# Kernel tuning notes

Hardware: AMD Instinct MI355X
Metric: run time of the kernel (lower is better)

The kernel has to match this reference:

```python
import jax, jax.numpy as jnp
import numpy as np

DIM = 768
NUM_HEADS = 12
HEAD_DIM = DIM // NUM_HEADS
SCALE = HEAD_DIM ** -0.5


def setup_inputs() -> dict:
    key = jax.random.key(0)
    k_x, k_qkv, k_pw, k_pb = jax.random.split(key, 4)
    x = jax.random.normal(k_x, (1, 4096, DIM), dtype=jnp.float32)
    # nn.Linear weights stored as [out, in]; apply as x @ W.T
    w_qkv = jax.random.normal(k_qkv, (3 * DIM, DIM), dtype=jnp.float32) * (DIM ** -0.5)
    w_proj = jax.random.normal(k_pw, (DIM, DIM), dtype=jnp.float32) * (DIM ** -0.5)
    b_proj = jax.random.normal(k_pb, (DIM,), dtype=jnp.float32) * 0.01
    return {"x": x, "w_qkv": w_qkv, "w_proj": w_proj, "b_proj": b_proj}


def reference(x, w_qkv, w_proj, b_proj):
    b, s, d = x.shape
    qkv = jnp.einsum('bsd,ed->bse', x, w_qkv)            # [B,S,3D]
    qkv = qkv.reshape(b, s, 3, NUM_HEADS, HEAD_DIM)
    qkv = jnp.transpose(qkv, (2, 0, 3, 1, 4))            # [3,B,H,S,hd]
    q, k, v = qkv[0], qkv[1], qkv[2]
    scores = jnp.einsum('bhqe,bhke->bhqk', q, k) * SCALE  # [B,H,S,S]
    probs = jax.nn.softmax(scores, axis=-1)
    attended = jnp.einsum('bhqk,bhke->bhqe', probs, v)    # [B,H,S,hd]
    attended = jnp.transpose(attended, (0, 2, 1, 3)).reshape(b, s, d)
    return jnp.einsum('bsd,ed->bse', attended, w_proj) + b_proj
```

## Files before the change

### kernel.cpp

```cpp
#include <hip/hip_runtime.h>
#include <hip/hip_bf16.h>

using short8 = __attribute__((ext_vector_type(8))) short;
using s16x4  = __attribute__((ext_vector_type(4))) short;
using f32x4  = __attribute__((ext_vector_type(4))) float;
using f32x16 = __attribute__((ext_vector_type(16))) float;
using v2i    = __attribute__((ext_vector_type(2))) int;

#define DIM   768
#define D3    2304
#define SEQL  4096
#define NHEAD 12
#define NSPLIT 2

#if defined(__has_builtin)
#  if __has_builtin(__builtin_amdgcn_permlane32_swap)
#    define HAVE_PLSWAP 1
#  endif
#endif

static __device__ __forceinline__ short f2bs(float f) {
  union { __hip_bfloat16 h; short s; } u;
  u.h = __float2bfloat16(f);
  return u.s;
}

static __device__ __forceinline__ float bf2f(short s) {
  union { unsigned u; float f; } x;
  x.u = ((unsigned)(unsigned short)s) << 16;
  return x.f;
}

static __device__ __forceinline__ int cvtpk(float lo, float hi) {
  int r;
  asm("v_cvt_pk_bf16_f32 %0, %1, %2" : "=v"(r) : "v"(lo), "v"(hi));
  return r;
}

static __device__ __forceinline__ float ex2(float x) {
  float r;
  asm("v_exp_f32 %0, %1" : "=v"(r) : "v"(x));
  return r;
}

static __device__ __forceinline__ void gl_lds16(const void* g, void* lds) {
  __builtin_amdgcn_global_load_lds((const __attribute__((address_space(1))) void*)g,
                                   (__attribute__((address_space(3))) void*)lds, 16, 0, 0);
}

__global__ __launch_bounds__(256) void cvt_kernel(const float* __restrict__ src,
                                                  short* __restrict__ dst,
                                                  int n, int nscaled) {
  int i = (blockIdx.x * 256 + threadIdx.x) * 4;
  if (i >= n) return;
  f32x4 v = *(const f32x4*)(src + i);
  float sc = (i < nscaled) ? 0.125f * 1.4426950408889634f : 1.0f;
  s16x4 o;
  #pragma unroll
  for (int j = 0; j < 4; ++j) o[j] = f2bs(v[j] * sc);
  *(s16x4*)(dst + i) = o;
}

template <bool BF16OUT>
__global__ __launch_bounds__(256) void gemm_bt(const short* __restrict__ A,
                                               const short* __restrict__ B,
                                               short* __restrict__ Cb,
                                               float* __restrict__ Cf,
                                               const float* __restrict__ bias,
                                               int M, int N, int K) {
  __shared__ short As[128 * 64];
  __shared__ short Bs[128 * 64];
  const int tid = threadIdx.x;
  const int l  = tid & 63;
  const int w  = tid >> 6;
  const int g  = l >> 4, lc = l & 15;
  const int wr = w >> 1, wc = w & 1;
  const int m0 = blockIdx.y * 128, n0 = blockIdx.x * 128;
  const int trow = tid >> 3;
  const int tcol = (tid & 7) * 8;

  f32x4 acc[4][4];
  #pragma unroll
  for (int a = 0; a < 4; ++a)
    #pragma unroll
    for (int b = 0; b < 4; ++b) acc[a][b] = (f32x4){0.f, 0.f, 0.f, 0.f};

  for (int k0 = 0; k0 < K; k0 += 64) {
    __syncthreads();
    #pragma unroll
    for (int i = 0; i < 4; ++i) {
      int row = i * 32 + trow;
      gl_lds16(A + (size_t)(m0 + row) * K + k0 + tcol, As + row * 64 + tcol);
      gl_lds16(B + (size_t)(n0 + row) * K + k0 + tcol, Bs + row * 64 + tcol);
    }
    __syncthreads();
    #pragma unroll
    for (int kk = 0; kk < 2; ++kk) {
      short8 af[4], bf[4];
      #pragma unroll
      for (int mt = 0; mt < 4; ++mt)
        af[mt] = *(const short8*)(As + (wr * 64 + mt * 16 + lc) * 64 + kk * 32 + g * 8);
      #pragma unroll
      for (int nt = 0; nt < 4; ++nt)
        bf[nt] = *(const short8*)(Bs + (wc * 64 + nt * 16 + lc) * 64 + kk * 32 + g * 8);
      #pragma unroll
      for (int mt = 0; mt < 4; ++mt)
        #pragma unroll
        for (int nt = 0; nt < 4; ++nt)
          acc[mt][nt] = __builtin_amdgcn_mfma_f32_16x16x32_bf16(af[mt], bf[nt], acc[mt][nt], 0, 0, 0);
    }
  }

  #pragma unroll
  for (int mt = 0; mt < 4; ++mt)
    #pragma unroll
    for (int nt = 0; nt < 4; ++nt)
      #pragma unroll
      for (int r = 0; r < 4; ++r) {
        int row = m0 + wr * 64 + mt * 16 + g * 4 + r;
        int col = n0 + wc * 64 + nt * 16 + lc;
        float v = acc[mt][nt][r];
        if (BF16OUT) Cb[(size_t)row * N + col] = f2bs(v);
        else         Cf[(size_t)row * N + col] = v + bias[col];
      }
}

__global__ __launch_bounds__(256) void transpose_v(const short* __restrict__ qkv,
                                                   short* __restrict__ vtg) {
  __shared__ short T[64][72];
  const int jt = blockIdx.x, hd = blockIdx.y, tid = threadIdx.x;
  #pragma unroll
  for (int i = 0; i < 2; ++i) {
    int idx = i * 256 + tid;
    int r = idx >> 3, c = idx & 7;
    *(short8*)&T[r][8 * c] =
        *(const short8*)(qkv + (size_t)(jt * 64 + r) * D3 + 1536 + hd * 64 + 8 * c);
  }
  __syncthreads();
  #pragma unroll
  for (int i = 0; i < 2; ++i) {
    int idx = i * 256 + tid;
    int d = idx >> 3, jc = idx & 7;
    short8 v;
    #pragma unroll
    for (int e = 0; e < 8; ++e) v[e] = T[8 * jc + e][d];
    *(short8*)(vtg + ((size_t)hd * 64 + d) * 4096 + jt * 64 + 8 * jc) = v;
  }
}

__global__ __launch_bounds__(256) void attn_kernel(const short* __restrict__ qkv,
                                                   const short* __restrict__ vtg,
                                                   short* __restrict__ O0,
                                                   short* __restrict__ O1,
                                                   float* __restrict__ Lp,
                                                   int tpb) {
  __shared__ short Ks[2][64 * 64];
  __shared__ short Vt[2][64 * 64];

  const int tid = threadIdx.x;
  const int l = tid & 63, w = tid >> 6;
  const int h = l >> 5;
  const int q5 = l & 31;
  const int head = blockIdx.y;
  const int hoff = head * 64;
  const int qbase = blockIdx.x * 128 + w * 32;
  const int z = blockIdx.z;
  const int t0 = z * tpb;

  short8 qf[4];
  {
    const short* qrow = qkv + (size_t)(qbase + q5) * D3 + hoff;
    #pragma unroll
    for (int ks = 0; ks < 4; ++ks) qf[ks] = *(const short8*)(qrow + ks * 16 + h * 8);
  }

  f32x16 o[2];
  #pragma unroll
  for (int nt = 0; nt < 2; ++nt)
    #pragma unroll
    for (int r = 0; r < 16; ++r) o[nt][r] = 0.f;
  float l_run = 0.f;

  const int swzK = 8 * (q5 & 7);

  #define STAGE_K(T, BUF)                                                        \
    {                                                                            \
      const int j0_ = (T) * 64;                                                  \
      _Pragma("unroll")                                                          \
      for (int i_ = 0; i_ < 2; ++i_) {                                           \
        int seg_ = i_ * 256 + tid;                                               \
        int row_ = seg_ >> 3, c_ = seg_ & 7;                                     \
        int d0_ = (8 * c_) ^ (8 * (row_ & 7));                                   \
        gl_lds16(qkv + (size_t)(j0_ + row_) * D3 + hoff + 768 + d0_,             \
                 &Ks[BUF][seg_ * 8]);                                            \
      }                                                                          \
    }
  #define STAGE_V(T, BUF)                                                        \
    {                                                                            \
      const int j0_ = (T) * 64;                                                  \
      _Pragma("unroll")                                                          \
      for (int i_ = 0; i_ < 2; ++i_) {                                           \
        int seg_ = i_ * 256 + tid;                                               \
        int d_ = seg_ >> 3, c_ = seg_ & 7;                                       \
        int joff_ = (8 * c_) ^ (8 * (d_ & 7));                                   \
        gl_lds16(vtg + ((size_t)hoff + d_) * 4096 + j0_ + joff_,                 \
                 &Vt[BUF][seg_ * 8]);                                            \
      }                                                                          \
    }

  STAGE_K(t0, 0);
  STAGE_V(t0, 0);
  asm volatile("s_waitcnt vmcnt(0)" ::: "memory");
  __syncthreads();

  for (int tt = 0; tt < tpb; ++tt) {
    const int t = t0 + tt;
    const int cur = tt & 1;
    const bool pre = (tt + 1 < tpb);
    if (pre) { STAGE_K(t + 1, cur ^ 1); STAGE_V(t + 1, cur ^ 1); }

    f32x16 p[2];
    #pragma unroll
    for (int mt = 0; mt < 2; ++mt)
      #pragma unroll
      for (int r = 0; r < 16; ++r) p[mt][r] = 0.f;
    __builtin_amdgcn_s_setprio(1);
    #pragma unroll
    for (int ks = 0; ks < 4; ++ks) {
      #pragma unroll
      for (int mt = 0; mt < 2; ++mt) {
        short8 kf = *(const short8*)(&Ks[cur][(mt * 32 + q5) * 64
                                              + ((ks * 16 + h * 8) ^ swzK)]);
        p[mt] = __builtin_amdgcn_mfma_f32_32x32x16_bf16(kf, qf[ks], p[mt], 0, 0, 0);
      }
    }
    __builtin_amdgcn_s_setprio(0);

    float sum = 0.f;
    #pragma unroll
    for (int mt = 0; mt < 2; ++mt)
      #pragma unroll
      for (int r = 0; r < 16; ++r) {
        float pe = ex2(p[mt][r]);
        p[mt][r] = pe;
        sum += pe;
      }
    l_run += sum;

    int D[16];
    #pragma unroll
    for (int mt = 0; mt < 2; ++mt)
      #pragma unroll
      for (int c = 0; c < 4; ++c) {
        D[mt * 8 + c * 2 + 0] = cvtpk(p[mt][4 * c + 0], p[mt][4 * c + 1]);
        D[mt * 8 + c * 2 + 1] = cvtpk(p[mt][4 * c + 2], p[mt][4 * c + 3]);
      }

    __builtin_amdgcn_s_setprio(1);
    #pragma unroll
    for (int ks = 0; ks < 4; ++ks) {
      union { int i[4]; short8 s; } pa;
#ifdef HAVE_PLSWAP
      v2i r02 = __builtin_amdgcn_permlane32_swap(D[4 * ks + 0], D[4 * ks + 2], false, false);
      v2i r13 = __builtin_amdgcn_permlane32_swap(D[4 * ks + 1], D[4 * ks + 3], false, false);
      pa.i[0] = r02[0];
      pa.i[1] = r13[0];
      pa.i[2] = r02[1];
      pa.i[3] = r13[1];
#else
      const bool hh = (h != 0);
      const int a0 = D[4 * ks + 0], a1 = D[4 * ks + 1];
      const int b0 = D[4 * ks + 2], b1 = D[4 * ks + 3];
      int snd0 = hh ? a0 : b0, snd1 = hh ? a1 : b1;
      int r0 = __shfl_xor(snd0, 32), r1 = __shfl_xor(snd1, 32);
      pa.i[0] = hh ? r0 : a0;
      pa.i[1] = hh ? r1 : a1;
      pa.i[2] = hh ? b0 : r0;
      pa.i[3] = hh ? b1 : r1;
#endif
      #pragma unroll
      for (int nt = 0; nt < 2; ++nt) {
        short8 vf = *(const short8*)(&Vt[cur][(nt * 32 + q5) * 64
                                              + ((ks * 16 + h * 8) ^ swzK)]);
        o[nt] = __builtin_amdgcn_mfma_f32_32x32x16_bf16(pa.s, vf, o[nt], 0, 0, 0);
      }
    }
    __builtin_amdgcn_s_setprio(0);

    asm volatile("s_waitcnt vmcnt(0)" ::: "memory");
    __syncthreads();
  }

  float l_tot = l_run + __shfl_xor(l_run, 32);
  if (h == 0) Lp[(size_t)z * SEQL * NHEAD + (qbase + q5) * NHEAD + head] = l_tot;
  short* Ob = (z == 0) ? O0 : O1;
  #pragma unroll
  for (int nt = 0; nt < 2; ++nt)
    #pragma unroll
    for (int pp = 0; pp < 4; ++pp)
      #pragma unroll
      for (int r = 0; r < 4; ++r) {
        int q = qbase + r + 8 * pp + 4 * h;
        int d = hoff + nt * 32 + q5;
        Ob[(size_t)q * DIM + d] = f2bs(o[nt][4 * pp + r]);
      }
}

__global__ __launch_bounds__(256) void combine_kernel(short* __restrict__ O0,
                                                      const short* __restrict__ O1,
                                                      const float* __restrict__ Lp) {
  int idx = blockIdx.x * 256 + threadIdx.x;
  int e0 = idx * 8;
  if (e0 >= SEQL * DIM) return;
  int q = e0 / DIM, col = e0 % DIM, head = col >> 6;
  float lv = Lp[q * NHEAD + head] + Lp[SEQL * NHEAD + q * NHEAD + head];
  float inv = 1.0f / lv;
  short8 a = *(const short8*)(O0 + e0);
  short8 b = *(const short8*)(O1 + e0);
  short8 r;
  #pragma unroll
  for (int j = 0; j < 8; ++j) r[j] = f2bs((bf2f(a[j]) + bf2f(b[j])) * inv);
  *(short8*)(O0 + e0) = r;
}

extern "C" void kernel_launch(void* const* d_in, const int* in_sizes, int n_in,
                              void* d_out, int out_size, void* d_ws, size_t ws_size,
                              hipStream_t stream) {
  (void)in_sizes; (void)n_in; (void)out_size; (void)ws_size;
  const float* x      = (const float*)d_in[0];
  const float* w_qkv  = (const float*)d_in[1];
  const float* w_proj = (const float*)d_in[2];
  const float* b_proj = (const float*)d_in[3];
  float* out = (float*)d_out;

  short* xb   = (short*)d_ws;
  short* wqb  = xb  + (size_t)SEQL * DIM;
  short* wpb  = wqb + (size_t)D3 * DIM;
  short* qkvb = wpb + (size_t)DIM * DIM;
  short* attb = qkvb + (size_t)SEQL * D3;
  short* Opart1 = xb;
  float* Lpart  = (float*)wqb;
  short* vtg    = (short*)d_out;

  cvt_kernel<<<SEQL * DIM / 1024, 256, 0, stream>>>(x, xb, SEQL * DIM, 0);
  cvt_kernel<<<D3 * DIM / 1024, 256, 0, stream>>>(w_qkv, wqb, D3 * DIM, DIM * DIM);
  cvt_kernel<<<DIM * DIM / 1024, 256, 0, stream>>>(w_proj, wpb, DIM * DIM, 0);

  gemm_bt<true ><<<dim3(D3 / 128, SEQL / 128), 256, 0, stream>>>(xb, wqb, qkvb, nullptr, nullptr, SEQL, D3, DIM);
  transpose_v<<<dim3(SEQL / 64, NHEAD), 256, 0, stream>>>(qkvb, vtg);
  attn_kernel<<<dim3(SEQL / 128, NHEAD, NSPLIT), 256, 0, stream>>>(qkvb, vtg, attb, Opart1, Lpart,
                                                                   (SEQL / 64) / NSPLIT);
  combine_kernel<<<SEQL * DIM / 8 / 256, 256, 0, stream>>>(attb, Opart1, Lpart);
  gemm_bt<false><<<dim3(DIM / 128, SEQL / 128), 256, 0, stream>>>(attb, wpb, nullptr, out, b_proj, SEQL, DIM, DIM);
}
```

Before: 152.4 us.

## Widen attention blocks to 8 waves, split KV three ways, fuse conversion kernels

The attention kernel now runs 512-thread blocks covering 256 queries, so each staged K/V tile is reused by twice as many waves, and each thread issues one K and one V load through incremented pointers. The KV sequence is split into three uneven chunks instead of two, with a third partial output buffer and a three-way combine. The three fp32-to-bf16 conversion launches are merged into one kernel. Smaller edits use a zero accumulator on the first MFMA instead of clearing registers, and a packed add for the row sum. The extra split adds combine traffic and another partial buffer, and the larger blocks may lower occupancy.

```diff
diff --git a/kernel.cpp b/kernel.cpp
--- a/kernel.cpp
+++ b/kernel.cpp
@@ -3,6 +3,7 @@
 
 using short8 = __attribute__((ext_vector_type(8))) short;
 using s16x4  = __attribute__((ext_vector_type(4))) short;
+using f32x2  = __attribute__((ext_vector_type(2))) float;
 using f32x4  = __attribute__((ext_vector_type(4))) float;
 using f32x16 = __attribute__((ext_vector_type(16))) float;
 using v2i    = __attribute__((ext_vector_type(2))) int;
@@ -11,7 +12,7 @@
 #define D3    2304
 #define SEQL  4096
 #define NHEAD 12
-#define NSPLIT 2
+#define NSPLIT 3
 
 #if defined(__has_builtin)
 #  if __has_builtin(__builtin_amdgcn_permlane32_swap)
@@ -37,6 +38,12 @@
   return r;
 }
 
+static __device__ __forceinline__ f32x2 pkadd(f32x2 a, f32x2 b) {
+  f32x2 r;
+  asm("v_pk_add_f32 %0, %1, %2" : "=v"(r) : "v"(a), "v"(b));
+  return r;
+}
+
 static __device__ __forceinline__ float ex2(float x) {
   float r;
   asm("v_exp_f32 %0, %1" : "=v"(r) : "v"(x));
@@ -48,13 +55,20 @@
                                    (__attribute__((address_space(3))) void*)lds, 16, 0, 0);
 }
 
-__global__ __launch_bounds__(256) void cvt_kernel(const float* __restrict__ src,
-                                                  short* __restrict__ dst,
-                                                  int n, int nscaled) {
-  int i = (blockIdx.x * 256 + threadIdx.x) * 4;
-  if (i >= n) return;
+__global__ __launch_bounds__(256) void cvt3_kernel(const float* __restrict__ x,
+                                                   const float* __restrict__ wq,
+                                                   const float* __restrict__ wp,
+                                                   short* __restrict__ xb,
+                                                   short* __restrict__ wqb,
+                                                   short* __restrict__ wpb) {
+  int b = blockIdx.x;
+  const float* src; short* dst; int base; float sc = 1.0f;
+  if (b < 3072)      { src = x;  dst = xb;  base = b * 1024; }
+  else if (b < 4800) { src = wq; dst = wqb; base = (b - 3072) * 1024;
+                       if (base < DIM * DIM) sc = 0.125f * 1.4426950408889634f; }
+  else               { src = wp; dst = wpb; base = (b - 4800) * 1024; }
+  int i = base + threadIdx.x * 4;
   f32x4 v = *(const f32x4*)(src + i);
-  float sc = (i < nscaled) ? 0.125f * 1.4426950408889634f : 1.0f;
   s16x4 o;
   #pragma unroll
   for (int j = 0; j < 4; ++j) o[j] = f2bs(v[j] * sc);
@@ -148,12 +162,12 @@
   }
 }
 
-__global__ __launch_bounds__(256) void attn_kernel(const short* __restrict__ qkv,
+__global__ __launch_bounds__(512) void attn_kernel(const short* __restrict__ qkv,
                                                    const short* __restrict__ vtg,
                                                    short* __restrict__ O0,
                                                    short* __restrict__ O1,
-                                                   float* __restrict__ Lp,
-                                                   int tpb) {
+                                                   short* __restrict__ O2,
+                                                   float* __restrict__ Lp) {
   __shared__ short Ks[2][64 * 64];
   __shared__ short Vt[2][64 * 64];
 
@@ -163,9 +177,9 @@
   const int q5 = l & 31;
   const int head = blockIdx.y;
   const int hoff = head * 64;
-  const int qbase = blockIdx.x * 128 + w * 32;
+  const int qbase = blockIdx.x * 256 + w * 32;
   const int z = blockIdx.z;
-  const int t0 = z * tpb;
+  const int t0 = (z * 64) / 3, tend = ((z + 1) * 64) / 3;
 
   short8 qf[4];
   {
@@ -180,50 +194,33 @@
     #pragma unroll
     for (int r = 0; r < 16; ++r) o[nt][r] = 0.f;
   float l_run = 0.f;
+  const f32x16 zacc = {};
 
   const int swzK = 8 * (q5 & 7);
 
-  #define STAGE_K(T, BUF)                                                        \
+  const int srow = tid >> 3, scol = (tid & 7) * 8;
+  const int sswz = 8 * (srow & 7);
+  const short* kptr = qkv + (size_t)(t0 * 64 + srow) * D3 + hoff + 768 + (scol ^ sswz);
+  const short* vptr = vtg + ((size_t)hoff + srow) * 4096 + t0 * 64 + (scol ^ sswz);
+
+  #define STAGE_KV(BUF)                                                          \
     {                                                                            \
-      const int j0_ = (T) * 64;                                                  \
-      _Pragma("unroll")                                                          \
-      for (int i_ = 0; i_ < 2; ++i_) {                                           \
-        int seg_ = i_ * 256 + tid;                                               \
-        int row_ = seg_ >> 3, c_ = seg_ & 7;                                     \
-        int d0_ = (8 * c_) ^ (8 * (row_ & 7));                                   \
-        gl_lds16(qkv + (size_t)(j0_ + row_) * D3 + hoff + 768 + d0_,             \
-                 &Ks[BUF][seg_ * 8]);                                            \
-      }                                                                          \
-    }
-  #define STAGE_V(T, BUF)                                                        \
-    {                                                                            \
-      const int j0_ = (T) * 64;                                                  \
-      _Pragma("unroll")                                                          \
-      for (int i_ = 0; i_ < 2; ++i_) {                                           \
-        int seg_ = i_ * 256 + tid;                                               \
-        int d_ = seg_ >> 3, c_ = seg_ & 7;                                       \
-        int joff_ = (8 * c_) ^ (8 * (d_ & 7));                                   \
-        gl_lds16(vtg + ((size_t)hoff + d_) * 4096 + j0_ + joff_,                 \
-                 &Vt[BUF][seg_ * 8]);                                            \
-      }                                                                          \
-    }
-
-  STAGE_K(t0, 0);
-  STAGE_V(t0, 0);
+      gl_lds16(kptr, &Ks[BUF][tid * 8]);                                         \
+      gl_lds16(vptr, &Vt[BUF][tid * 8]);                                         \
+      kptr += 64 * D3;                                                           \
+      vptr += 64;                                                                \
+    }
+
+  STAGE_KV(0);
   asm volatile("s_waitcnt vmcnt(0)" ::: "memory");
   __syncthreads();
 
-  for (int tt = 0; tt < tpb; ++tt) {
-    const int t = t0 + tt;
-    const int cur = tt & 1;
-    const bool pre = (tt + 1 < tpb);
-    if (pre) { STAGE_K(t + 1, cur ^ 1); STAGE_V(t + 1, cur ^ 1); }
+  for (int tt = t0; tt < tend; ++tt) {
+    const int cur = (tt - t0) & 1;
+    const bool pre = (tt + 1 < tend);
+    if (pre) STAGE_KV(cur ^ 1);
 
     f32x16 p[2];
-    #pragma unroll
-    for (int mt = 0; mt < 2; ++mt)
-      #pragma unroll
-      for (int r = 0; r < 16; ++r) p[mt][r] = 0.f;
     __builtin_amdgcn_s_setprio(1);
     #pragma unroll
     for (int ks = 0; ks < 4; ++ks) {
@@ -231,21 +228,24 @@
       for (int mt = 0; mt < 2; ++mt) {
         short8 kf = *(const short8*)(&Ks[cur][(mt * 32 + q5) * 64
                                               + ((ks * 16 + h * 8) ^ swzK)]);
-        p[mt] = __builtin_amdgcn_mfma_f32_32x32x16_bf16(kf, qf[ks], p[mt], 0, 0, 0);
+        p[mt] = __builtin_amdgcn_mfma_f32_32x32x16_bf16(kf, qf[ks],
+                                                        ks == 0 ? zacc : p[mt], 0, 0, 0);
       }
     }
     __builtin_amdgcn_s_setprio(0);
 
-    float sum = 0.f;
+    f32x2 s2 = {0.f, 0.f};
     #pragma unroll
     for (int mt = 0; mt < 2; ++mt)
       #pragma unroll
-      for (int r = 0; r < 16; ++r) {
-        float pe = ex2(p[mt][r]);
-        p[mt][r] = pe;
-        sum += pe;
-      }
-    l_run += sum;
+      for (int i = 0; i < 8; ++i) {
+        float pe0 = ex2(p[mt][2 * i]);
+        float pe1 = ex2(p[mt][2 * i + 1]);
+        p[mt][2 * i] = pe0;
+        p[mt][2 * i + 1] = pe1;
+        s2 = pkadd(s2, (f32x2){pe0, pe1});
+      }
+    l_run += s2[0] + s2[1];
 
     int D[16];
     #pragma unroll
@@ -293,7 +293,7 @@
 
   float l_tot = l_run + __shfl_xor(l_run, 32);
   if (h == 0) Lp[(size_t)z * SEQL * NHEAD + (qbase + q5) * NHEAD + head] = l_tot;
-  short* Ob = (z == 0) ? O0 : O1;
+  short* Ob = (z == 0) ? O0 : (z == 1) ? O1 : O2;
   #pragma unroll
   for (int nt = 0; nt < 2; ++nt)
     #pragma unroll
@@ -308,18 +308,22 @@
 
 __global__ __launch_bounds__(256) void combine_kernel(short* __restrict__ O0,
                                                       const short* __restrict__ O1,
+                                                      const short* __restrict__ O2,
                                                       const float* __restrict__ Lp) {
   int idx = blockIdx.x * 256 + threadIdx.x;
   int e0 = idx * 8;
   if (e0 >= SEQL * DIM) return;
   int q = e0 / DIM, col = e0 % DIM, head = col >> 6;
-  float lv = Lp[q * NHEAD + head] + Lp[SEQL * NHEAD + q * NHEAD + head];
+  int i0 = q * NHEAD + head;
+  float lv = Lp[i0] + Lp[SEQL * NHEAD + i0] + Lp[2 * SEQL * NHEAD + i0];
   float inv = 1.0f / lv;
   short8 a = *(const short8*)(O0 + e0);
   short8 b = *(const short8*)(O1 + e0);
+  short8 c = *(const short8*)(O2 + e0);
   short8 r;
   #pragma unroll
-  for (int j = 0; j < 8; ++j) r[j] = f2bs((bf2f(a[j]) + bf2f(b[j])) * inv);
+  for (int j = 0; j < 8; ++j)
+    r[j] = f2bs((bf2f(a[j]) + bf2f(b[j]) + bf2f(c[j])) * inv);
   *(short8*)(O0 + e0) = r;
 }
 
@@ -341,15 +345,12 @@
   short* Opart1 = xb;
   float* Lpart  = (float*)wqb;
   short* vtg    = (short*)d_out;
-
-  cvt_kernel<<<SEQL * DIM / 1024, 256, 0, stream>>>(x, xb, SEQL * DIM, 0);
-  cvt_kernel<<<D3 * DIM / 1024, 256, 0, stream>>>(w_qkv, wqb, D3 * DIM, DIM * DIM);
-  cvt_kernel<<<DIM * DIM / 1024, 256, 0, stream>>>(w_proj, wpb, DIM * DIM, 0);
-
+  short* Opart2 = vtg + (size_t)SEQL * DIM;
+
+  cvt3_kernel<<<5376, 256, 0, stream>>>(x, w_qkv, w_proj, xb, wqb, wpb);
   gemm_bt<true ><<<dim3(D3 / 128, SEQL / 128), 256, 0, stream>>>(xb, wqb, qkvb, nullptr, nullptr, SEQL, D3, DIM);
   transpose_v<<<dim3(SEQL / 64, NHEAD), 256, 0, stream>>>(qkvb, vtg);
-  attn_kernel<<<dim3(SEQL / 128, NHEAD, NSPLIT), 256, 0, stream>>>(qkvb, vtg, attb, Opart1, Lpart,
-                                                                   (SEQL / 64) / NSPLIT);
-  combine_kernel<<<SEQL * DIM / 8 / 256, 256, 0, stream>>>(attb, Opart1, Lpart);
+  attn_kernel<<<dim3(SEQL / 256, NHEAD, NSPLIT), 512, 0, stream>>>(qkvb, vtg, attb, Opart1, Opart2, Lpart);
+  combine_kernel<<<SEQL * DIM / 8 / 256, 256, 0, stream>>>(attb, Opart1, Opart2, Lpart);
   gemm_bt<false><<<dim3(DIM / 128, SEQL / 128), 256, 0, stream>>>(attb, wpb, nullptr, out, b_proj, SEQL, DIM, DIM);
 }
```

Result: slower. 156.4 us (+2.6%).
